# Kernel tuning notes

Hardware: AMD Instinct MI355X
Metric: run time of the kernel (lower is better)

Reference implementation:

```python
import jax, jax.numpy as jnp
import numpy as np

EPS = 1e-5

def conv2d(x, w, stride=1, padding=0, bias=None):
    out = jax.lax.conv_general_dilated(
        x, w, (stride, stride), [(padding, padding), (padding, padding)],
        dimension_numbers=('NCHW', 'OIHW', 'NCHW'))
    if bias is not None:
        out = out + bias[None, :, None, None]
    return out

def bn_relu(x, gamma, beta, mean, var):
    scale = gamma / jnp.sqrt(var + EPS)
    return jax.nn.relu(x * scale[None, :, None, None]
                       + (beta - mean * scale)[None, :, None, None])

def deform_conv(x, wp, bp, wc, ks, pad, stride):
    # Canonical DeformConv2d (v1, modulation=False) from pytorch-deform-conv-v2.
    b, c, H, W = x.shape
    N = ks * ks
    offset = conv2d(x, wp, stride=stride, padding=1, bias=bp)        # (b,2N,h,w)
    h, w = offset.shape[2], offset.shape[3]
    xp = jnp.pad(x, ((0, 0), (0, 0), (pad, pad), (pad, pad)))        # zero_padding
    Hp, Wp = H + 2 * pad, W + 2 * pad
    off = offset.transpose(0, 2, 3, 1)                               # (b,h,w,2N)
    rng = jnp.arange(-(ks - 1) // 2, (ks - 1) // 2 + 1, dtype=x.dtype)
    pnx, pny = jnp.meshgrid(rng, rng, indexing='ij')
    pnx, pny = pnx.reshape(-1), pny.reshape(-1)                      # (N,)
    p0x = jnp.arange(1, h * stride + 1, stride, dtype=x.dtype)       # torch starts at 1
    p0y = jnp.arange(1, w * stride + 1, stride, dtype=x.dtype)
    px = p0x[None, :, None, None] + pnx[None, None, None, :] + off[..., :N]  # (b,h,w,N)
    py = p0y[None, None, :, None] + pny[None, None, None, :] + off[..., N:]
    qx0 = jnp.floor(jax.lax.stop_gradient(px))
    qy0 = jnp.floor(jax.lax.stop_gradient(py))
    qx0c = jnp.clip(qx0, 0, Hp - 1).astype(jnp.int32)
    qx1c = jnp.clip(qx0 + 1, 0, Hp - 1).astype(jnp.int32)
    qy0c = jnp.clip(qy0, 0, Wp - 1).astype(jnp.int32)
    qy1c = jnp.clip(qy0 + 1, 0, Wp - 1).astype(jnp.int32)
    pxc = jnp.clip(px, 0, Hp - 1)
    pyc = jnp.clip(py, 0, Wp - 1)
    fx0 = qx0c.astype(x.dtype); fx1 = qx1c.astype(x.dtype)
    fy0 = qy0c.astype(x.dtype); fy1 = qy1c.astype(x.dtype)
    g_lt = (1 + (fx0 - pxc)) * (1 + (fy0 - pyc))
    g_rb = (1 - (fx1 - pxc)) * (1 - (fy1 - pyc))
    g_lb = (1 + (fx0 - pxc)) * (1 - (fy1 - pyc))
    g_rt = (1 - (fx1 - pxc)) * (1 + (fy0 - pyc))
    xf = xp.reshape(b, c, Hp * Wp)
    def gather(qx, qy):
        idx = (qx * Wp + qy).reshape(b, 1, h * w * N)
        return jnp.take_along_axis(xf, idx, axis=2).reshape(b, c, h, w, N)
    x_off = (g_lt[:, None] * gather(qx0c, qy0c)
             + g_rb[:, None] * gather(qx1c, qy1c)
             + g_lb[:, None] * gather(qx0c, qy1c)
             + g_rt[:, None] * gather(qx1c, qy0c))                   # (b,c,h,w,N)
    # stride=ks conv over the reshaped (h*ks, w*ks) map == einsum over sample slot n
    return jnp.einsum('bchwn,ocn->bohw', x_off, wc.reshape(wc.shape[0], c, N))

def setup_inputs() -> dict:
    key = jax.random.key(0)
    ks = iter(jax.random.split(key, 40))
    def nrm(shape, scale):
        return jax.random.normal(next(ks), shape, dtype=jnp.float32) * scale
    def he(shape):  # fan_in = prod of all but first dim
        return nrm(shape, float(np.sqrt(2.0 / np.prod(shape[1:]))))
    def bn(c):
        return (jnp.ones((c,), jnp.float32) + nrm((c,), 0.05),  # gamma
                nrm((c,), 0.05),                                 # beta
                nrm((c,), 0.1),                                  # running mean
                jax.random.uniform(next(ks), (c,), jnp.float32, 0.5, 1.5))  # var
    inp = {'x': jax.random.normal(next(ks), (256, 3, 32, 32), dtype=jnp.float32)}
    inp['w1'] = he((32, 3, 3, 3)); inp['b1'] = nrm((32,), 0.01)
    inp['g1'], inp['be1'], inp['m1'], inp['v1'] = bn(32)
    inp['wp2'] = nrm((18, 32, 3, 3), 0.01); inp['bp2'] = nrm((18,), 0.001)
    inp['wc2'] = he((64, 32, 3, 3))
    inp['g2'], inp['be2'], inp['m2'], inp['v2'] = bn(64)
    inp['wp3'] = nrm((18, 64, 3, 3), 0.01); inp['bp3'] = nrm((18,), 0.001)
    inp['wc3'] = he((128, 64, 3, 3))
    inp['g3'], inp['be3'], inp['m3'], inp['v3'] = bn(128)
    inp['wp4'] = nrm((18, 128, 3, 3), 0.01); inp['bp4'] = nrm((18,), 0.001)
    inp['wc4'] = he((128, 128, 3, 3))
    inp['g4'], inp['be4'], inp['m4'], inp['v4'] = bn(128)
    inp['wcls'] = nrm((100, 128), float(1.0 / np.sqrt(128)))
    inp['bcls'] = nrm((100,), 0.01)
    return inp

def reference(x, w1, b1, g1, be1, m1, v1,
              wp2, bp2, wc2, g2, be2, m2, v2,
              wp3, bp3, wc3, g3, be3, m3, v3,
              wp4, bp4, wc4, g4, be4, m4, v4,
              wcls, bcls):
    h = bn_relu(conv2d(x, w1, stride=1, padding=1, bias=b1), g1, be1, m1, v1)   # (b,32,32,32)
    h = bn_relu(deform_conv(h, wp2, bp2, wc2, 3, 1, 2), g2, be2, m2, v2)        # (b,64,16,16)
    h = bn_relu(deform_conv(h, wp3, bp3, wc3, 3, 1, 1), g3, be3, m3, v3)        # (b,128,16,16)
    h = bn_relu(deform_conv(h, wp4, bp4, wc4, 3, 1, 2), g4, be4, m4, v4)        # (b,128,8,8)
    h = jnp.mean(h, axis=(2, 3))                                                # avg_pool2d(8) -> (b,128)
    return h @ wcls.T + bcls[None, :]
```

## Files before the change

### kernel.cpp

```cpp
#include <hip/hip_runtime.h>
#include <math.h>

#define BN_EPS 1e-5f

typedef __attribute__((ext_vector_type(4))) float f4;
typedef __attribute__((ext_vector_type(4))) int i4v;
typedef __attribute__((ext_vector_type(8))) short short8;
typedef __attribute__((ext_vector_type(4))) float f32x4;

__device__ inline unsigned short f2bf(float f) {
    unsigned int u = __builtin_bit_cast(unsigned int, f);
    return (unsigned short)((u + 0x7FFFu + ((u >> 16) & 1u)) >> 16);
}
__device__ inline float blo(int u) { return __builtin_bit_cast(float, (int)(u << 16)); }
__device__ inline float bhi(int u) { return __builtin_bit_cast(float, (int)(u & 0xffff0000)); }
__device__ inline int pkbf_fast(float hi, float lo) {
    unsigned uh = __builtin_bit_cast(unsigned, hi) + 0x8000u;
    unsigned ul = __builtin_bit_cast(unsigned, lo) + 0x8000u;
    return (int)__builtin_amdgcn_perm(uh, ul, 0x07060302u);
}

struct CvtSeg { const float* src; unsigned short* dst; int oreal, c, kpad, end; };
struct CvtArgs { CvtSeg s[7]; };

__global__ __launch_bounds__(256)
void cvt_all(CvtArgs a)
{
    int idx = blockIdx.x * 256 + threadIdx.x;
    int base = 0;
    #pragma unroll
    for (int i = 0; i < 7; ++i) {
        if (idx < a.s[i].end) {
            int local = idx - base;
            int kpad = a.s[i].kpad, c = a.s[i].c;
            int o = local / kpad, k = local - o * kpad;
            unsigned short val = 0;
            if (o < a.s[i].oreal && k < 9 * c) {
                int n = k / c, cc = k - n * c;
                val = f2bf(a.s[i].src[(o * c + cc) * 9 + n]);
            }
            a.s[i].dst[local] = val;
            return;
        }
        base = a.s[i].end;
    }
}

__global__ __launch_bounds__(256)
void conv1_tile(const float* __restrict__ x, const unsigned short* __restrict__ wq,
                const float* __restrict__ bias, const float* __restrict__ g,
                const float* __restrict__ be, const float* __restrict__ m,
                const float* __restrict__ v, unsigned short* __restrict__ out)
{
    __shared__ __align__(16) float img[3072];
    __shared__ __align__(16) unsigned short wt[32 * 40];
    __shared__ float scb[32], shb[32];
    const int tid = threadIdx.x;
    const int b = blockIdx.x >> 2;
    const int qtr = blockIdx.x & 3;
    if (tid < 32) {
        float sc = g[tid] * rsqrtf(v[tid] + BN_EPS);
        scb[tid] = sc;
        shb[tid] = be[tid] - m[tid] * sc + bias[tid] * sc;
    }
    *(ushort4*)&wt[(tid >> 3) * 40 + (tid & 7) * 4] =
        *(const ushort4*)(wq + (tid >> 3) * 32 + (tid & 7) * 4);
    const float* xb = x + (size_t)b * 3072;
    #pragma unroll
    for (int r = 0; r < 3; ++r) {
        int idx = r * 256 + tid;
        *(f4*)&img[idx * 4] = *(const f4*)(xb + idx * 4);
    }
    __syncthreads();
    const int wid = tid >> 6, lane = tid & 63, quad = lane >> 4, m16 = lane & 15;
    short8 af0 = *(const short8*)&wt[m16 * 40 + quad * 8];
    short8 af1 = *(const short8*)&wt[(16 + m16) * 40 + quad * 8];
    #pragma unroll
    for (int it = 0; it < 4; ++it) {
        int pix = qtr * 256 + it * 64 + wid * 16 + m16;
        int i = pix >> 5, j = pix & 31;
        short8 bfrag;
        #pragma unroll
        for (int jj = 0; jj < 8; ++jj) {
            int k = quad * 8 + jj;
            float val = 0.f;
            if (k < 27) {
                int n = k / 3, c = k - n * 3;
                int u = i - 1 + n / 3, vv = j - 1 + n % 3;
                if (u >= 0 && u < 32 && vv >= 0 && vv < 32)
                    val = img[c * 1024 + u * 32 + vv];
            }
            bfrag[jj] = (short)f2bf(val);
        }
        f32x4 a0 = {0.f,0.f,0.f,0.f}, a1 = {0.f,0.f,0.f,0.f};
        a0 = __builtin_amdgcn_mfma_f32_16x16x32_bf16(af0, bfrag, a0, 0, 0, 0);
        a1 = __builtin_amdgcn_mfma_f32_16x16x32_bf16(af1, bfrag, a1, 0, 0, 0);
        unsigned short* op = out + ((size_t)b * 1024 + pix) * 32;
        ushort4 s0, s1;
        #pragma unroll
        for (int rr = 0; rr < 4; ++rr) {
            int o0 = quad * 4 + rr, o1 = 16 + quad * 4 + rr;
            ((unsigned short*)&s0)[rr] = f2bf(fmaxf(fmaf(a0[rr], scb[o0], shb[o0]), 0.f));
            ((unsigned short*)&s1)[rr] = f2bf(fmaxf(fmaf(a1[rr], scb[o1], shb[o1]), 0.f));
        }
        *(ushort4*)(op + quad * 4) = s0;
        *(ushort4*)(op + 16 + quad * 4) = s1;
    }
}

template<int C, int OREAL, int OPAD, int H, int W, int OH, int OW, int S,
         int MTILE, bool DEF, bool BN>
__global__ __launch_bounds__(256, DEF ? 3 : 4)
void dconv(const unsigned short* __restrict__ xact, const float* __restrict__ offp,
           const unsigned short* __restrict__ wq,
           const float* __restrict__ q0, const float* __restrict__ q1,
           const float* __restrict__ q2, const float* __restrict__ q3,
           void* __restrict__ outv)
{
    constexpr int K = C * 9;
    constexpr int KCH = C / 32;
    constexpr int OSPLIT = (OPAD >= 64) ? 4 : 2;
    constexpr int G = 4 / OSPLIT;
    constexpr int OT = OPAD / (16 * OSPLIT);
    constexpr int PW = MTILE / G;
    constexpr int ST = PW / 16;
    constexpr int CP = C + 8;
    constexpr int GL = C / 8;
    constexpr int NGRP = 256 / GL;
    constexpr int NT_ITER = MTILE / NGRP;
    constexpr int OHW = OH * OW;
    constexpr int HWC = H * W * C;
    constexpr int Hp = H + 2, Wp = W + 2;
    static_assert(PW % 16 == 0 && OT >= 1 && MTILE % NGRP == 0, "tiling");

    __shared__ __align__(16) unsigned short xo[2][MTILE * CP];
    __shared__ __align__(16) i4v tab_i[DEF ? MTILE : 1][9];
    __shared__ __align__(16) f4  tab_w[DEF ? MTILE : 1][9];
    __shared__ int tab_o[DEF ? 1 : MTILE][9];
    __shared__ int tab_m[DEF ? 1 : MTILE][9];
    __shared__ int imgb[MTILE];
    __shared__ float scb[OPAD], shb[OPAD];

    const int tid = threadIdx.x;
    const int p0 = blockIdx.x * MTILE;

    if (tid < MTILE) imgb[tid] = ((p0 + tid) / OHW) * HWC;
    if (BN) {
        for (int o = tid; o < OREAL; o += 256) {
            float sc = q0[o] * rsqrtf(q3[o] + BN_EPS);
            scb[o] = sc;
            shb[o] = q1[o] - q2[o] * sc;
        }
    } else {
        for (int o = tid; o < OREAL; o += 256) scb[o] = q0[o];
    }

    for (int e = tid; e < MTILE * 9; e += 256) {
        int lp = e / 9, n = e % 9;
        int p = p0 + lp;
        int rem = p % OHW;
        int i = rem / OW, j = rem % OW;
        if constexpr (DEF) {
            float ox = offp[(size_t)p * 18 + n];
            float oy = offp[(size_t)p * 18 + 9 + n];
            float px = (float)(i * S + n / 3) + ox;
            float py = (float)(j * S + n % 3) + oy;
            int qx0 = (int)floorf(px), qy0 = (int)floorf(py);
            int x0 = min(max(qx0, 0), Hp - 1), x1 = min(max(qx0 + 1, 0), Hp - 1);
            int y0 = min(max(qy0, 0), Wp - 1), y1 = min(max(qy0 + 1, 0), Wp - 1);
            float pxc = fminf(fmaxf(px, 0.f), (float)(Hp - 1));
            float pyc = fminf(fmaxf(py, 0.f), (float)(Wp - 1));
            float gx0 = 1.f + ((float)x0 - pxc), gx1 = 1.f - ((float)x1 - pxc);
            float gy0 = 1.f + ((float)y0 - pyc), gy1 = 1.f - ((float)y1 - pyc);
            int u0 = x0 - 1, u1 = x1 - 1, v0 = y0 - 1, v1 = y1 - 1;
            bool k0 = (u0 >= 0 && u0 < H && v0 >= 0 && v0 < W);
            bool k1 = (u1 >= 0 && u1 < H && v1 >= 0 && v1 < W);
            bool k2 = (u0 >= 0 && u0 < H && v1 >= 0 && v1 < W);
            bool k3 = (u1 >= 0 && u1 < H && v0 >= 0 && v0 < W);
            i4v ti; f4 tw;
            ti[0] = k0 ? (u0 * W + v0) * C : 0;  tw[0] = k0 ? gx0 * gy0 : 0.f;
            ti[1] = k1 ? (u1 * W + v1) * C : 0;  tw[1] = k1 ? gx1 * gy1 : 0.f;
            ti[2] = k2 ? (u0 * W + v1) * C : 0;  tw[2] = k2 ? gx0 * gy1 : 0.f;
            ti[3] = k3 ? (u1 * W + v0) * C : 0;  tw[3] = k3 ? gx1 * gy0 : 0.f;
            tab_i[lp][n] = ti;
            tab_w[lp][n] = tw;
        } else {
            int u = i * S - 1 + n / 3, vv = j * S - 1 + n % 3;
            bool ok = (u >= 0 && u < H && vv >= 0 && vv < W);
            tab_o[lp][n] = ok ? (u * W + vv) * C : 0;
            tab_m[lp][n] = ok ? -1 : 0;
        }
    }

    const int gl = tid % GL;
    const int grp = tid / GL;
    const int wid = tid >> 6, lane = tid & 63, quad = lane >> 4, m16 = lane & 15;
    const int og = wid % OSPLIT, pg = wid / OSPLIT;
    const int obase = og * OT * 16;
    const int pixbase = pg * PW;

    i4v T[NT_ITER][DEF ? 4 : 1];

    auto gather_issue = [&](int n) {
        #pragma unroll
        for (int it = 0; it < NT_ITER; ++it) {
            const int pix = it * NGRP + grp;
            const unsigned short* xb = xact + imgb[pix] + gl * 8;
            if constexpr (DEF) {
                i4v ti = tab_i[pix][n];
                T[it][0] = *(const i4v*)(xb + ti[0]);
                T[it][1] = *(const i4v*)(xb + ti[1]);
                T[it][2] = *(const i4v*)(xb + ti[2]);
                T[it][3] = *(const i4v*)(xb + ti[3]);
            } else {
                T[it][0] = *(const i4v*)(xb + tab_o[pix][n]);
            }
        }
    };
    auto gather_commit = [&](int n, int buf) {
        #pragma unroll
        for (int it = 0; it < NT_ITER; ++it) {
            const int pix = it * NGRP + grp;
            i4v R;
            if constexpr (DEF) {
                f4 tw = tab_w[pix][n];
                #pragma unroll
                for (int e2 = 0; e2 < 4; ++e2) {
                    float lo = tw[0] * blo(T[it][0][e2]);
                    lo = fmaf(tw[1], blo(T[it][1][e2]), lo);
                    lo = fmaf(tw[2], blo(T[it][2][e2]), lo);
                    lo = fmaf(tw[3], blo(T[it][3][e2]), lo);
                    float hi = tw[0] * bhi(T[it][0][e2]);
                    hi = fmaf(tw[1], bhi(T[it][1][e2]), hi);
                    hi = fmaf(tw[2], bhi(T[it][2][e2]), hi);
                    hi = fmaf(tw[3], bhi(T[it][3][e2]), hi);
                    R[e2] = pkbf_fast(hi, lo);
                }
            } else {
                int mask = tab_m[pix][n];
                #pragma unroll
                for (int e2 = 0; e2 < 4; ++e2) R[e2] = T[it][0][e2] & mask;
            }
            *(i4v*)&xo[buf][pix * CP + gl * 8] = R;
        }
    };

    auto load_wf = [&](int n, short8 (*wf)[OT]) {
        #pragma unroll
        for (int ch = 0; ch < KCH; ++ch)
            #pragma unroll
            for (int t = 0; t < OT; ++t)
                wf[ch][t] = *(const short8*)(wq + (size_t)(obase + t * 16 + m16) * K
                                             + n * C + ch * 32 + quad * 8);
    };

    f32x4 acc[ST][OT];
    #pragma unroll
    for (int st = 0; st < ST; ++st)
        #pragma unroll
        for (int t = 0; t < OT; ++t) acc[st][t] = (f32x4){0.f, 0.f, 0.f, 0.f};

    short8 wfA[KCH][OT], wfB[KCH][OT];
    __syncthreads();
    gather_issue(0);
    load_wf(0, wfA);
    gather_commit(0, 0);
    __syncthreads();

    for (int n = 0; n < 9; ++n) {
        const int cur = n & 1;
        if (n < 8) {
            gather_issue(n + 1);
            load_wf(n + 1, wfB);
        }
        #pragma unroll
        for (int ch = 0; ch < KCH; ++ch)
            #pragma unroll
            for (int st = 0; st < ST; ++st) {
                short8 bf = *(const short8*)&xo[cur][(pixbase + st * 16 + m16) * CP
                                                    + ch * 32 + quad * 8];
                #pragma unroll
                for (int t = 0; t < OT; ++t)
                    acc[st][t] = __builtin_amdgcn_mfma_f32_16x16x32_bf16(
                        wfA[ch][t], bf, acc[st][t], 0, 0, 0);
            }
        if (n < 8) {
            gather_commit(n + 1, cur ^ 1);
            #pragma unroll
            for (int ch = 0; ch < KCH; ++ch)
                #pragma unroll
                for (int t = 0; t < OT; ++t) wfA[ch][t] = wfB[ch][t];
        }
        __syncthreads();
    }

    if constexpr (BN) {
        unsigned short* outw = (unsigned short*)outv;
        #pragma unroll
        for (int st = 0; st < ST; ++st) {
            const int p = p0 + pixbase + st * 16 + m16;
            #pragma unroll
            for (int t = 0; t < OT; ++t) {
                int o = obase + t * 16 + quad * 4;
                ushort4 s;
                #pragma unroll
                for (int rr = 0; rr < 4; ++rr)
                    ((unsigned short*)&s)[rr] =
                        f2bf(fmaxf(fmaf(acc[st][t][rr], scb[o + rr], shb[o + rr]), 0.f));
                *(ushort4*)(outw + (size_t)p * OPAD + o) = s;
            }
        }
    } else {
        float* outf = (float*)outv;
        #pragma unroll
        for (int st = 0; st < ST; ++st) {
            const int p = p0 + pixbase + st * 16 + m16;
            #pragma unroll
            for (int t = 0; t < OT; ++t)
                #pragma unroll
                for (int rr = 0; rr < 4; ++rr) {
                    int o = obase + t * 16 + quad * 4 + rr;
                    if (o < OREAL)
                        outf[(size_t)p * 18 + o] = acc[st][t][rr] + scb[o];
                }
        }
    }
}

__global__ __launch_bounds__(128)
void pool_fc(const unsigned short* __restrict__ h4, const float* __restrict__ wcls,
             const float* __restrict__ bcls, float* __restrict__ out)
{
    __shared__ float pool[128];
    int b = blockIdx.x;
    int tid = threadIdx.x;
    const unsigned short* src = h4 + (size_t)b * 8192;
    float s = 0.f;
    #pragma unroll
    for (int t = 0; t < 64; ++t)
        s += __builtin_bit_cast(float, (unsigned)src[t * 128 + tid] << 16);
    pool[tid] = s * (1.f / 64.f);
    __syncthreads();
    if (tid < 100) {
        float acc = bcls[tid];
        const float* wr = wcls + tid * 128;
        #pragma unroll
        for (int c = 0; c < 128; ++c) acc = fmaf(pool[c], wr[c], acc);
        out[(size_t)b * 100 + tid] = acc;
    }
}

extern "C" void kernel_launch(void* const* d_in, const int* in_sizes, int n_in,
                              void* d_out, int out_size, void* d_ws, size_t ws_size,
                              hipStream_t stream)
{
    const float* x    = (const float*)d_in[0];
    const float* w1   = (const float*)d_in[1];
    const float* b1   = (const float*)d_in[2];
    const float* g1   = (const float*)d_in[3];
    const float* be1  = (const float*)d_in[4];
    const float* m1   = (const float*)d_in[5];
    const float* v1   = (const float*)d_in[6];
    const float* wp2  = (const float*)d_in[7];
    const float* bp2  = (const float*)d_in[8];
    const float* wc2  = (const float*)d_in[9];
    const float* g2   = (const float*)d_in[10];
    const float* be2  = (const float*)d_in[11];
    const float* m2   = (const float*)d_in[12];
    const float* v2   = (const float*)d_in[13];
    const float* wp3  = (const float*)d_in[14];
    const float* bp3  = (const float*)d_in[15];
    const float* wc3  = (const float*)d_in[16];
    const float* g3   = (const float*)d_in[17];
    const float* be3  = (const float*)d_in[18];
    const float* m3   = (const float*)d_in[19];
    const float* v3   = (const float*)d_in[20];
    const float* wp4  = (const float*)d_in[21];
    const float* bp4  = (const float*)d_in[22];
    const float* wc4  = (const float*)d_in[23];
    const float* g4   = (const float*)d_in[24];
    const float* be4  = (const float*)d_in[25];
    const float* m4   = (const float*)d_in[26];
    const float* v4   = (const float*)d_in[27];
    const float* wcls = (const float*)d_in[28];
    const float* bcls = (const float*)d_in[29];
    float* out = (float*)d_out;

    float* ws  = (float*)d_ws;
    float* off = ws;
    unsigned short* h1 = (unsigned short*)(off + 1179648);
    unsigned short* h2 = h1 + 8388608;
    unsigned short* h3 = h2 + 4194304;
    unsigned short* h4 = h3 + 8388608;
    unsigned short* wc2b = h4 + 2097152;
    unsigned short* wc3b = wc2b + 18432;
    unsigned short* wc4b = wc3b + 73728;
    unsigned short* wp2b = wc4b + 147456;
    unsigned short* wp3b = wp2b + 9216;
    unsigned short* wp4b = wp3b + 18432;
    unsigned short* wq1  = wp4b + 36864;
    (void)ws_size; (void)in_sizes; (void)n_in; (void)out_size;

    CvtArgs ca;
    ca.s[0] = { wc2, wc2b, 64, 32, 288, 18432 };
    ca.s[1] = { wc3, wc3b, 128, 64, 576, 92160 };
    ca.s[2] = { wc4, wc4b, 128, 128, 1152, 239616 };
    ca.s[3] = { wp2, wp2b, 18, 32, 288, 248832 };
    ca.s[4] = { wp3, wp3b, 18, 64, 576, 267264 };
    ca.s[5] = { wp4, wp4b, 18, 128, 1152, 304128 };
    ca.s[6] = { w1, wq1, 32, 3, 32, 305152 };
    cvt_all<<<1192, 256, 0, stream>>>(ca);

    conv1_tile<<<1024, 256, 0, stream>>>(x, wq1, b1, g1, be1, m1, v1, h1);

    dconv<32, 18, 32, 32, 32, 16, 16, 2, 64, false, false><<<1024, 256, 0, stream>>>(
        h1, nullptr, wp2b, bp2, nullptr, nullptr, nullptr, off);
    dconv<32, 64, 64, 32, 32, 16, 16, 2, 64, true, true><<<1024, 256, 0, stream>>>(
        h1, off, wc2b, g2, be2, m2, v2, h2);

    dconv<64, 18, 32, 16, 16, 16, 16, 1, 64, false, false><<<1024, 256, 0, stream>>>(
        h2, nullptr, wp3b, bp3, nullptr, nullptr, nullptr, off);
    dconv<64, 128, 128, 16, 16, 16, 16, 1, 64, true, true><<<1024, 256, 0, stream>>>(
        h2, off, wc3b, g3, be3, m3, v3, h3);

    dconv<128, 18, 32, 16, 16, 8, 8, 2, 32, false, false><<<512, 256, 0, stream>>>(
        h3, nullptr, wp4b, bp4, nullptr, nullptr, nullptr, off);
    dconv<128, 128, 128, 16, 16, 8, 8, 2, 32, true, true><<<512, 256, 0, stream>>>(
        h3, off, wc4b, g4, be4, m4, v4, h4);

    pool_fc<<<256, 128, 0, stream>>>(h4, wcls, bcls, out);
}
```

Before: 239.8 us.

## Fuse offset convolution into deformable convolution kernel per layer

```diff
diff --git a/kernel.cpp b/kernel.cpp
--- a/kernel.cpp
+++ b/kernel.cpp
@@ -108,36 +108,36 @@
     }
 }
 
-template<int C, int OREAL, int OPAD, int H, int W, int OH, int OW, int S,
-         int MTILE, bool DEF, bool BN>
-__global__ __launch_bounds__(256, DEF ? 3 : 4)
-void dconv(const unsigned short* __restrict__ xact, const float* __restrict__ offp,
-           const unsigned short* __restrict__ wq,
-           const float* __restrict__ q0, const float* __restrict__ q1,
-           const float* __restrict__ q2, const float* __restrict__ q3,
-           void* __restrict__ outv)
+template<int C, int OREAL, int OPAD, int H, int W, int OH, int OW, int S, int MTILE>
+__global__ __launch_bounds__(256, 3)
+void dconv_fused(const unsigned short* __restrict__ xact,
+                 const unsigned short* __restrict__ wp, const float* __restrict__ bp,
+                 const unsigned short* __restrict__ wc,
+                 const float* __restrict__ g, const float* __restrict__ be,
+                 const float* __restrict__ m, const float* __restrict__ v,
+                 unsigned short* __restrict__ out)
 {
     constexpr int K = C * 9;
     constexpr int KCH = C / 32;
-    constexpr int OSPLIT = (OPAD >= 64) ? 4 : 2;
-    constexpr int G = 4 / OSPLIT;
-    constexpr int OT = OPAD / (16 * OSPLIT);
-    constexpr int PW = MTILE / G;
-    constexpr int ST = PW / 16;
+    constexpr int OT = OPAD / 64;
+    constexpr int ST = MTILE / 16;
+    constexpr int PWP = MTILE / 2;
+    constexpr int STP = PWP / 16;
     constexpr int CP = C + 8;
     constexpr int GL = C / 8;
     constexpr int NGRP = 256 / GL;
-    constexpr int NT_ITER = MTILE / NGRP;
+    constexpr int NT = MTILE / NGRP;
     constexpr int OHW = OH * OW;
     constexpr int HWC = H * W * C;
-    constexpr int Hp = H + 2, Wp = W + 2;
-    static_assert(PW % 16 == 0 && OT >= 1 && MTILE % NGRP == 0, "tiling");
+    constexpr int Hp = H + 2, Wpp = W + 2;
+    static_assert(MTILE % NGRP == 0 && OPAD % 64 == 0, "tiling");
 
     __shared__ __align__(16) unsigned short xo[2][MTILE * CP];
-    __shared__ __align__(16) i4v tab_i[DEF ? MTILE : 1][9];
-    __shared__ __align__(16) f4  tab_w[DEF ? MTILE : 1][9];
-    __shared__ int tab_o[DEF ? 1 : MTILE][9];
-    __shared__ int tab_m[DEF ? 1 : MTILE][9];
+    __shared__ __align__(16) i4v tab_i[MTILE][9];
+    __shared__ __align__(16) f4  tab_w[MTILE][9];
+    __shared__ int tab_o[MTILE][9];
+    __shared__ int tab_m[MTILE][9];
+    __shared__ float off_lds[MTILE][20];
     __shared__ int imgb[MTILE];
     __shared__ float scb[OPAD], shb[OPAD];
 
@@ -145,85 +145,146 @@
     const int p0 = blockIdx.x * MTILE;
 
     if (tid < MTILE) imgb[tid] = ((p0 + tid) / OHW) * HWC;
-    if (BN) {
-        for (int o = tid; o < OREAL; o += 256) {
-            float sc = q0[o] * rsqrtf(q3[o] + BN_EPS);
-            scb[o] = sc;
-            shb[o] = q1[o] - q2[o] * sc;
-        }
-    } else {
-        for (int o = tid; o < OREAL; o += 256) scb[o] = q0[o];
-    }
-
+    for (int o = tid; o < OREAL; o += 256) {
+        float sc = g[o] * rsqrtf(v[o] + BN_EPS);
+        scb[o] = sc;
+        shb[o] = be[o] - m[o] * sc;
+    }
     for (int e = tid; e < MTILE * 9; e += 256) {
         int lp = e / 9, n = e % 9;
         int p = p0 + lp;
         int rem = p % OHW;
         int i = rem / OW, j = rem % OW;
-        if constexpr (DEF) {
-            float ox = offp[(size_t)p * 18 + n];
-            float oy = offp[(size_t)p * 18 + 9 + n];
-            float px = (float)(i * S + n / 3) + ox;
-            float py = (float)(j * S + n % 3) + oy;
-            int qx0 = (int)floorf(px), qy0 = (int)floorf(py);
-            int x0 = min(max(qx0, 0), Hp - 1), x1 = min(max(qx0 + 1, 0), Hp - 1);
-            int y0 = min(max(qy0, 0), Wp - 1), y1 = min(max(qy0 + 1, 0), Wp - 1);
-            float pxc = fminf(fmaxf(px, 0.f), (float)(Hp - 1));
-            float pyc = fminf(fmaxf(py, 0.f), (float)(Wp - 1));
-            float gx0 = 1.f + ((float)x0 - pxc), gx1 = 1.f - ((float)x1 - pxc);
-            float gy0 = 1.f + ((float)y0 - pyc), gy1 = 1.f - ((float)y1 - pyc);
-            int u0 = x0 - 1, u1 = x1 - 1, v0 = y0 - 1, v1 = y1 - 1;
-            bool k0 = (u0 >= 0 && u0 < H && v0 >= 0 && v0 < W);
-            bool k1 = (u1 >= 0 && u1 < H && v1 >= 0 && v1 < W);
-            bool k2 = (u0 >= 0 && u0 < H && v1 >= 0 && v1 < W);
-            bool k3 = (u1 >= 0 && u1 < H && v0 >= 0 && v0 < W);
-            i4v ti; f4 tw;
-            ti[0] = k0 ? (u0 * W + v0) * C : 0;  tw[0] = k0 ? gx0 * gy0 : 0.f;
-            ti[1] = k1 ? (u1 * W + v1) * C : 0;  tw[1] = k1 ? gx1 * gy1 : 0.f;
-            ti[2] = k2 ? (u0 * W + v1) * C : 0;  tw[2] = k2 ? gx0 * gy1 : 0.f;
-            ti[3] = k3 ? (u1 * W + v0) * C : 0;  tw[3] = k3 ? gx1 * gy0 : 0.f;
-            tab_i[lp][n] = ti;
-            tab_w[lp][n] = tw;
-        } else {
-            int u = i * S - 1 + n / 3, vv = j * S - 1 + n % 3;
-            bool ok = (u >= 0 && u < H && vv >= 0 && vv < W);
-            tab_o[lp][n] = ok ? (u * W + vv) * C : 0;
-            tab_m[lp][n] = ok ? -1 : 0;
-        }
-    }
-
-    const int gl = tid % GL;
-    const int grp = tid / GL;
+        int u = i * S - 1 + n / 3, vv = j * S - 1 + n % 3;
+        bool ok = (u >= 0 && u < H && vv >= 0 && vv < W);
+        tab_o[lp][n] = ok ? (u * W + vv) * C : 0;
+        tab_m[lp][n] = ok ? -1 : 0;
+    }
+    __syncthreads();
+
+    const int gl = tid % GL, grp = tid / GL;
     const int wid = tid >> 6, lane = tid & 63, quad = lane >> 4, m16 = lane & 15;
-    const int og = wid % OSPLIT, pg = wid / OSPLIT;
-    const int obase = og * OT * 16;
-    const int pixbase = pg * PW;
-
-    i4v T[NT_ITER][DEF ? 4 : 1];
-
-    auto gather_issue = [&](int n) {
-        #pragma unroll
-        for (int it = 0; it < NT_ITER; ++it) {
-            const int pix = it * NGRP + grp;
-            const unsigned short* xb = xact + imgb[pix] + gl * 8;
-            if constexpr (DEF) {
+
+    {
+        const int ogp = wid & 1, pgp = wid >> 1;
+        const int obp = ogp * 16;
+        const int pbp = pgp * PWP;
+        i4v Tp[NT];
+        auto issueA = [&](int n) {
+            #pragma unroll
+            for (int it = 0; it < NT; ++it) {
+                const int pix = it * NGRP + grp;
+                Tp[it] = *(const i4v*)(xact + imgb[pix] + gl * 8 + tab_o[pix][n]);
+            }
+        };
+        auto commitA = [&](int n, int buf) {
+            #pragma unroll
+            for (int it = 0; it < NT; ++it) {
+                const int pix = it * NGRP + grp;
+                int mask = tab_m[pix][n];
+                i4v R;
+                #pragma unroll
+                for (int e2 = 0; e2 < 4; ++e2) R[e2] = Tp[it][e2] & mask;
+                *(i4v*)&xo[buf][pix * CP + gl * 8] = R;
+            }
+        };
+        auto loadWp = [&](int n, short8* wf) {
+            #pragma unroll
+            for (int ch = 0; ch < KCH; ++ch)
+                wf[ch] = *(const short8*)(wp + (size_t)(obp + m16) * K
+                                          + n * C + ch * 32 + quad * 8);
+        };
+        f32x4 accp[STP];
+        #pragma unroll
+        for (int st = 0; st < STP; ++st) accp[st] = (f32x4){0.f, 0.f, 0.f, 0.f};
+        short8 wfA[KCH], wfB[KCH];
+        issueA(0);
+        loadWp(0, wfA);
+        commitA(0, 0);
+        __syncthreads();
+        for (int n = 0; n < 9; ++n) {
+            const int cur = n & 1;
+            if (n < 8) { issueA(n + 1); loadWp(n + 1, wfB); }
+            #pragma unroll
+            for (int ch = 0; ch < KCH; ++ch)
+                #pragma unroll
+                for (int st = 0; st < STP; ++st) {
+                    short8 bf = *(const short8*)&xo[cur][(pbp + st * 16 + m16) * CP
+                                                        + ch * 32 + quad * 8];
+                    accp[st] = __builtin_amdgcn_mfma_f32_16x16x32_bf16(
+                        wfA[ch], bf, accp[st], 0, 0, 0);
+                }
+            if (n < 8) {
+                commitA(n + 1, cur ^ 1);
+                #pragma unroll
+                for (int ch = 0; ch < KCH; ++ch) wfA[ch] = wfB[ch];
+            }
+            __syncthreads();
+        }
+        #pragma unroll
+        for (int st = 0; st < STP; ++st) {
+            int pix = pbp + st * 16 + m16;
+            #pragma unroll
+            for (int rr = 0; rr < 4; ++rr) {
+                int o = obp + quad * 4 + rr;
+                if (o < 18) off_lds[pix][o] = accp[st][rr] + bp[o];
+            }
+        }
+    }
+    __syncthreads();
+
+    for (int e = tid; e < MTILE * 9; e += 256) {
+        int lp = e / 9, n = e % 9;
+        int p = p0 + lp;
+        int rem = p % OHW;
+        int i = rem / OW, j = rem % OW;
+        float ox = off_lds[lp][n];
+        float oy = off_lds[lp][9 + n];
+        float px = (float)(i * S + n / 3) + ox;
+        float py = (float)(j * S + n % 3) + oy;
+        int qx0 = (int)floorf(px), qy0 = (int)floorf(py);
+        int x0 = min(max(qx0, 0), Hp - 1), x1 = min(max(qx0 + 1, 0), Hp - 1);
+        int y0 = min(max(qy0, 0), Wpp - 1), y1 = min(max(qy0 + 1, 0), Wpp - 1);
+        float pxc = fminf(fmaxf(px, 0.f), (float)(Hp - 1));
+        float pyc = fminf(fmaxf(py, 0.f), (float)(Wpp - 1));
+        float gx0 = 1.f + ((float)x0 - pxc), gx1 = 1.f - ((float)x1 - pxc);
+        float gy0 = 1.f + ((float)y0 - pyc), gy1 = 1.f - ((float)y1 - pyc);
+        int u0 = x0 - 1, u1 = x1 - 1, v0 = y0 - 1, v1 = y1 - 1;
+        bool k0 = (u0 >= 0 && u0 < H && v0 >= 0 && v0 < W);
+        bool k1 = (u1 >= 0 && u1 < H && v1 >= 0 && v1 < W);
+        bool k2 = (u0 >= 0 && u0 < H && v1 >= 0 && v1 < W);
+        bool k3 = (u1 >= 0 && u1 < H && v0 >= 0 && v0 < W);
+        i4v ti; f4 tw;
+        ti[0] = k0 ? (u0 * W + v0) * C : 0;  tw[0] = k0 ? gx0 * gy0 : 0.f;
+        ti[1] = k1 ? (u1 * W + v1) * C : 0;  tw[1] = k1 ? gx1 * gy1 : 0.f;
+        ti[2] = k2 ? (u0 * W + v1) * C : 0;  tw[2] = k2 ? gx0 * gy1 : 0.f;
+        ti[3] = k3 ? (u1 * W + v0) * C : 0;  tw[3] = k3 ? gx1 * gy0 : 0.f;
+        tab_i[lp][n] = ti;
+        tab_w[lp][n] = tw;
+    }
+    __syncthreads();
+
+    {
+        const int obase = wid * OT * 16;
+        i4v T[NT][4];
+        auto issueC = [&](int n) {
+            #pragma unroll
+            for (int it = 0; it < NT; ++it) {
+                const int pix = it * NGRP + grp;
+                const unsigned short* xb = xact + imgb[pix] + gl * 8;
                 i4v ti = tab_i[pix][n];
                 T[it][0] = *(const i4v*)(xb + ti[0]);
                 T[it][1] = *(const i4v*)(xb + ti[1]);
                 T[it][2] = *(const i4v*)(xb + ti[2]);
                 T[it][3] = *(const i4v*)(xb + ti[3]);
-            } else {
-                T[it][0] = *(const i4v*)(xb + tab_o[pix][n]);
-            }
-        }
-    };
-    auto gather_commit = [&](int n, int buf) {
-        #pragma unroll
-        for (int it = 0; it < NT_ITER; ++it) {
-            const int pix = it * NGRP + grp;
-            i4v R;
-            if constexpr (DEF) {
+            }
+        };
+        auto commitC = [&](int n, int buf) {
+            #pragma unroll
+            for (int it = 0; it < NT; ++it) {
+                const int pix = it * NGRP + grp;
                 f4 tw = tab_w[pix][n];
+                i4v R;
                 #pragma unroll
                 for (int e2 = 0; e2 < 4; ++e2) {
                     float lo = tw[0] * blo(T[it][0][e2]);
@@ -236,69 +297,60 @@
                     hi = fmaf(tw[3], bhi(T[it][3][e2]), hi);
                     R[e2] = pkbf_fast(hi, lo);
                 }
-            } else {
-                int mask = tab_m[pix][n];
-                #pragma unroll
-                for (int e2 = 0; e2 < 4; ++e2) R[e2] = T[it][0][e2] & mask;
-            }
-            *(i4v*)&xo[buf][pix * CP + gl * 8] = R;
-        }
-    };
-
-    auto load_wf = [&](int n, short8 (*wf)[OT]) {
-        #pragma unroll
-        for (int ch = 0; ch < KCH; ++ch)
-            #pragma unroll
-            for (int t = 0; t < OT; ++t)
-                wf[ch][t] = *(const short8*)(wq + (size_t)(obase + t * 16 + m16) * K
-                                             + n * C + ch * 32 + quad * 8);
-    };
-
-    f32x4 acc[ST][OT];
-    #pragma unroll
-    for (int st = 0; st < ST; ++st)
-        #pragma unroll
-        for (int t = 0; t < OT; ++t) acc[st][t] = (f32x4){0.f, 0.f, 0.f, 0.f};
-
-    short8 wfA[KCH][OT], wfB[KCH][OT];
-    __syncthreads();
-    gather_issue(0);
-    load_wf(0, wfA);
-    gather_commit(0, 0);
-    __syncthreads();
-
-    for (int n = 0; n < 9; ++n) {
-        const int cur = n & 1;
-        if (n < 8) {
-            gather_issue(n + 1);
-            load_wf(n + 1, wfB);
-        }
-        #pragma unroll
-        for (int ch = 0; ch < KCH; ++ch)
-            #pragma unroll
-            for (int st = 0; st < ST; ++st) {
-                short8 bf = *(const short8*)&xo[cur][(pixbase + st * 16 + m16) * CP
-                                                    + ch * 32 + quad * 8];
+                *(i4v*)&xo[buf][pix * CP + gl * 8] = R;
+            }
+        };
+        auto loadWc = [&](int n, short8 (*wf)[OT]) {
+            #pragma unroll
+            for (int ch = 0; ch < KCH; ++ch)
                 #pragma unroll
                 for (int t = 0; t < OT; ++t)
-                    acc[st][t] = __builtin_amdgcn_mfma_f32_16x16x32_bf16(
-                        wfA[ch][t], bf, acc[st][t], 0, 0, 0);
-            }
-        if (n < 8) {
-            gather_commit(n + 1, cur ^ 1);
+                    wf[ch][t] = *(const short8*)(wc + (size_t)(obase + t * 16 + m16) * K
+                                                 + n * C + ch * 32 + quad * 8);
+        };
+
+        f32x4 acc[ST][OT];
+        #pragma unroll
+        for (int st = 0; st < ST; ++st)
+            #pragma unroll
+            for (int t = 0; t < OT; ++t) acc[st][t] = (f32x4){0.f, 0.f, 0.f, 0.f};
+
+        short8 wfA[KCH][OT], wfB[KCH][OT];
+        issueC(0);
+        loadWc(0, wfA);
+        commitC(0, 0);
+        __syncthreads();
+
+        for (int n = 0; n < 9; ++n) {
+            const int cur = n & 1;
+            if (n < 8) {
+                issueC(n + 1);
+                loadWc(n + 1, wfB);
+            }
             #pragma unroll
             for (int ch = 0; ch < KCH; ++ch)
                 #pragma unroll
-                for (int t = 0; t < OT; ++t) wfA[ch][t] = wfB[ch][t];
-        }
-        __syncthreads();
-    }
-
-    if constexpr (BN) {
-        unsigned short* outw = (unsigned short*)outv;
+                for (int st = 0; st < ST; ++st) {
+                    short8 bf = *(const short8*)&xo[cur][(st * 16 + m16) * CP
+                                                        + ch * 32 + quad * 8];
+                    #pragma unroll
+                    for (int t = 0; t < OT; ++t)
+                        acc[st][t] = __builtin_amdgcn_mfma_f32_16x16x32_bf16(
+                            wfA[ch][t], bf, acc[st][t], 0, 0, 0);
+                }
+            if (n < 8) {
+                commitC(n + 1, cur ^ 1);
+                #pragma unroll
+                for (int ch = 0; ch < KCH; ++ch)
+                    #pragma unroll
+                    for (int t = 0; t < OT; ++t) wfA[ch][t] = wfB[ch][t];
+            }
+            __syncthreads();
+        }
+
         #pragma unroll
         for (int st = 0; st < ST; ++st) {
-            const int p = p0 + pixbase + st * 16 + m16;
+            const int p = p0 + st * 16 + m16;
             #pragma unroll
             for (int t = 0; t < OT; ++t) {
                 int o = obase + t * 16 + quad * 4;
@@ -307,22 +359,8 @@
                 for (int rr = 0; rr < 4; ++rr)
                     ((unsigned short*)&s)[rr] =
                         f2bf(fmaxf(fmaf(acc[st][t][rr], scb[o + rr], shb[o + rr]), 0.f));
-                *(ushort4*)(outw + (size_t)p * OPAD + o) = s;
-            }
-        }
-    } else {
-        float* outf = (float*)outv;
-        #pragma unroll
-        for (int st = 0; st < ST; ++st) {
-            const int p = p0 + pixbase + st * 16 + m16;
-            #pragma unroll
-            for (int t = 0; t < OT; ++t)
-                #pragma unroll
-                for (int rr = 0; rr < 4; ++rr) {
-                    int o = obase + t * 16 + quad * 4 + rr;
-                    if (o < OREAL)
-                        outf[(size_t)p * 18 + o] = acc[st][t][rr] + scb[o];
-                }
+                *(ushort4*)(out + (size_t)p * OPAD + o) = s;
+            }
         }
     }
 }
@@ -386,9 +424,7 @@
     const float* bcls = (const float*)d_in[29];
     float* out = (float*)d_out;
 
-    float* ws  = (float*)d_ws;
-    float* off = ws;
-    unsigned short* h1 = (unsigned short*)(off + 1179648);
+    unsigned short* h1 = (unsigned short*)d_ws;
     unsigned short* h2 = h1 + 8388608;
     unsigned short* h3 = h2 + 4194304;
     unsigned short* h4 = h3 + 8388608;
@@ -413,20 +449,14 @@
 
     conv1_tile<<<1024, 256, 0, stream>>>(x, wq1, b1, g1, be1, m1, v1, h1);
 
-    dconv<32, 18, 32, 32, 32, 16, 16, 2, 64, false, false><<<1024, 256, 0, stream>>>(
-        h1, nullptr, wp2b, bp2, nullptr, nullptr, nullptr, off);
-    dconv<32, 64, 64, 32, 32, 16, 16, 2, 64, true, true><<<1024, 256, 0, stream>>>(
-        h1, off, wc2b, g2, be2, m2, v2, h2);
-
-    dconv<64, 18, 32, 16, 16, 16, 16, 1, 64, false, false><<<1024, 256, 0, stream>>>(
-        h2, nullptr, wp3b, bp3, nullptr, nullptr, nullptr, off);
-    dconv<64, 128, 128, 16, 16, 16, 16, 1, 64, true, true><<<1024, 256, 0, stream>>>(
-        h2, off, wc3b, g3, be3, m3, v3, h3);
-
-    dconv<128, 18, 32, 16, 16, 8, 8, 2, 32, false, false><<<512, 256, 0, stream>>>(
-        h3, nullptr, wp4b, bp4, nullptr, nullptr, nullptr, off);
-    dconv<128, 128, 128, 16, 16, 8, 8, 2, 32, true, true><<<512, 256, 0, stream>>>(
-        h3, off, wc4b, g4, be4, m4, v4, h4);
+    dconv_fused<32, 64, 64, 32, 32, 16, 16, 2, 64><<<1024, 256, 0, stream>>>(
+        h1, wp2b, bp2, wc2b, g2, be2, m2, v2, h2);
+
+    dconv_fused<64, 128, 128, 16, 16, 16, 16, 1, 64><<<1024, 256, 0, stream>>>(
+        h2, wp3b, bp3, wc3b, g3, be3, m3, v3, h3);
+
+    dconv_fused<128, 128, 128, 16, 16, 8, 8, 2, 32><<<512, 256, 0, stream>>>(
+        h3, wp4b, bp4, wc4b, g4, be4, m4, v4, h4);
 
     pool_fc<<<256, 128, 0, stream>>>(h4, wcls, bcls, out);
 }
```

Result: faster. 234.0 us, median of 2 (-2.4%).
